# Performance work log

Hardware: AMD Instinct MI355X
Metric: run time of the kernel (lower is better)

The kernel has to match this reference:

```python
import jax, jax.numpy as jnp
import numpy as np

P = 32      # process_dim (event types)
H = 1024    # hidden_size
T = 128     # sequence length
B = 128     # batch size


def setup_inputs() -> dict:
    key = jax.random.key(0)
    k_dt, k_ty, k_e, k_w, k_b = jax.random.split(key, 5)
    seq_dt = jax.random.uniform(k_dt, (T, B), dtype=jnp.float32)
    seq_types = jax.random.randint(k_ty, (T, B), 0, P, dtype=jnp.int32)
    h0 = jnp.zeros((B, H), jnp.float32)
    c0 = jnp.zeros((B, H), jnp.float32)
    # Embedding: P+1 rows, padding row (index P) zeroed as in nn.Embedding(padding_idx=P)
    embed = (jax.random.normal(k_e, (P + 1, P), jnp.float32) * 0.02).at[P].set(0.0)
    # 7 gate Linears fused into one weight: order = [input, forget, output,
    # input_target, forget_target, z, decay]; torch Linear is y = v @ W^T + b,
    # here W is stored pre-transposed as [P+H, 7H].
    W = jax.random.normal(k_w, (P + H, 7 * H), jnp.float32) / np.sqrt(P + H)
    b = jax.random.normal(k_b, (7 * H,), jnp.float32) * 0.01
    return {"seq_dt": seq_dt, "seq_types": seq_types, "h0": h0, "c0": c0,
            "embed": embed, "W": W, "b": b}


def reference(seq_dt, seq_types, h0, c0, embed, W, b):
    def step(carry, inp):
        h_t, c_t, c_tgt = carry
        dt, types = inp                       # dt: [B], types: [B]
        x = embed[types]                      # [B, P]
        v = jnp.concatenate([x, h_t], axis=1) # [B, P+H]
        g = v @ W + b                         # fused 7-gate GEMM -> [B, 7H]
        gi, gf, go, git, gft, gz, gd = jnp.split(g, 7, axis=1)
        inpt = jax.nn.sigmoid(gi)
        forget = jax.nn.sigmoid(gf)
        output = jax.nn.sigmoid(go)
        in_tgt = jax.nn.sigmoid(git)
        fg_tgt = jax.nn.sigmoid(gft)
        z = jnp.tanh(gz)
        decay = jax.nn.softplus(8.0 * gd) / 8.0  # Softplus(beta=8)
        c_i = forget * c_t + inpt * z
        h_i = output * jnp.tanh(c_i)
        c_tgt_new = fg_tgt * c_tgt + in_tgt * z
        c_new = c_tgt_new + (c_i - c_tgt_new) * jnp.exp(-decay * dt[:, None])
        h_new = output * jnp.tanh(c_new)
        return (h_new, c_new, c_tgt_new), (h_i, h_new, output, c_i, c_tgt_new, decay)

    _, ys = jax.lax.scan(step, (h0, c0, c0), (seq_dt, seq_types))
    hiddens, hiddens_decayed, outputs, cells, cell_targets, decays = ys
    return hiddens, hiddens_decayed, outputs, cells, cell_targets, decays
```

## Files before the change

### kernel.cpp

```cpp
#include <hip/hip_runtime.h>
#include <hip/hip_bf16.h>

#define TT 128
#define BB 128
#define HH 1024
#define PP 32
#define G7 7168

typedef __attribute__((ext_vector_type(8))) short short8;
typedef __attribute__((ext_vector_type(4))) float f32x4;

__device__ __forceinline__ ushort f2bf(float f) {
    union { float f; unsigned int u; } v; v.f = f;
    unsigned int u = v.u;
    return (ushort)((u + 0x7FFFu + ((u >> 16) & 1u)) >> 16);
}
__device__ __forceinline__ float sigm(float x) { return 1.f / (1.f + __expf(-x)); }
__device__ __forceinline__ float ftanh(float x) {
    float e = __expf(2.f * x);
    return 1.f - 2.f / (e + 1.f);
}

__global__ void prep_w2(const float* __restrict__ W, ushort* __restrict__ W2) {
    int nt = blockIdx.x;
    int ki = blockIdx.y;
    int lane = threadIdx.x;
    int n = nt * 16 + (lane & 15);
    int k = ki * 32 + (lane >> 4) * 8;
    size_t off = ((size_t)(nt * 32 + ki) * 64 + lane) * 8;
    #pragma unroll
    for (int e = 0; e < 8; ++e)
        W2[off + e] = f2bf(W[(size_t)(32 + k + e) * G7 + n]);
}

__global__ void prep_g0(const float* __restrict__ W, const float* __restrict__ embed,
                        const float* __restrict__ bias, float* __restrict__ G0) {
    int n = blockIdx.x * 256 + threadIdx.x;
    int ty = blockIdx.y;
    float acc = bias[n];
    for (int p = 0; p < PP; ++p)
        acc += embed[ty * PP + p] * W[(size_t)p * G7 + n];
    G0[(size_t)ty * G7 + n] = acc;
}

__global__ void prep_init(const float* __restrict__ h0, const float* __restrict__ c0,
                          ushort* __restrict__ A4, float* __restrict__ c_state,
                          float* __restrict__ ctgt_state) {
    int i = blockIdx.x * 256 + threadIdx.x;
    int b = i >> 10, k = i & 1023;
    int lane = (b & 15) | (((k >> 3) & 3) << 4);
    size_t off = ((size_t)(((b >> 5) * 32 + (k >> 5)) * 2 + ((b >> 4) & 1)) * 64 + lane) * 8 + (k & 7);
    A4[off] = f2bf(h0[i]);
    c_state[i] = c0[i];
    ctgt_state[i] = c0[i];
}

__global__ __launch_bounds__(896) void step_kernel(
    const ushort* __restrict__ W2, const float* __restrict__ G0,
    const float* __restrict__ dts, const int* __restrict__ types,
    const ushort* __restrict__ a_read, ushort* __restrict__ a_write,
    float* __restrict__ c_state, float* __restrict__ ctgt_state,
    float* __restrict__ out, int t)
{
    __shared__ short8 Albuf[4096];
    __shared__ f32x4 pbuf[7][2][64];
    __shared__ float gbuf[7][32][16];
    const int tid = threadIdx.x;
    const int wave = tid >> 6, lane = tid & 63;
    const int g = wave >> 1, kh = wave & 1;
    const int bid = blockIdx.x;
    const int ht = (bid & 7) * 8 + ((bid >> 3) & 7);
    const int bq = bid >> 6;

    const short8* Asrc = reinterpret_cast<const short8*>(a_read) + bq * 4096;
    #pragma unroll
    for (int r = 0; r < 4; ++r)
        Albuf[r * 896 + tid] = Asrc[r * 896 + tid];
    if (tid < 512) Albuf[3584 + tid] = Asrc[3584 + tid];
    __syncthreads();

    const short8* Wv = reinterpret_cast<const short8*>(W2)
                     + (size_t)(g * 64 + ht) * 2048 + (kh * 16) * 64 + lane;
    const short8* As = Albuf + (kh * 16) * 2 * 64 + lane;
    f32x4 acc0 = {}, acc1 = {};
    #pragma unroll 8
    for (int j = 0; j < 16; ++j) {
        short8 wf = Wv[j * 64];
        short8 a0 = As[(j * 2 + 0) * 64];
        short8 a1 = As[(j * 2 + 1) * 64];
        acc0 = __builtin_amdgcn_mfma_f32_16x16x32_bf16(a0, wf, acc0, 0, 0, 0);
        acc1 = __builtin_amdgcn_mfma_f32_16x16x32_bf16(a1, wf, acc1, 0, 0, 0);
    }

    if (kh == 1) { pbuf[g][0][lane] = acc0; pbuf[g][1][lane] = acc1; }
    __syncthreads();
    if (kh == 0) {
        acc0 += pbuf[g][0][lane];
        acc1 += pbuf[g][1][lane];
        const int rb = (lane >> 4) * 4, lr = lane & 15;
        #pragma unroll
        for (int r = 0; r < 4; ++r) {
            gbuf[g][rb + r][lr]      = acc0[r];
            gbuf[g][16 + rb + r][lr] = acc1[r];
        }
    }
    __syncthreads();

    if (tid < 512) {
        const int br = tid >> 4, hc = tid & 15;
        const int b = bq * 32 + br;
        const int h = ht * 16 + hc;
        const int ty = types[t * BB + b];
        const float dt = dts[t * BB + b];
        const float* g0p = G0 + (size_t)ty * G7 + h;
        float pre[7];
        #pragma unroll
        for (int gg = 0; gg < 7; ++gg)
            pre[gg] = gbuf[gg][br][hc] + g0p[gg * HH];

        float inpt   = sigm(pre[0]);
        float forget = sigm(pre[1]);
        float output = sigm(pre[2]);
        float itg    = sigm(pre[3]);
        float ftg    = sigm(pre[4]);
        float z      = ftanh(pre[5]);
        float x8     = 8.f * pre[6];
        float sp     = fmaxf(x8, 0.f) + __logf(1.f + __expf(-fabsf(x8)));
        float decay  = sp * 0.125f;

        const size_t si = (size_t)b * HH + h;
        float c    = c_state[si];
        float ctgt = ctgt_state[si];
        float c_i      = forget * c + inpt * z;
        float h_i      = output * ftanh(c_i);
        float ctgt_new = ftg * ctgt + itg * z;
        float edt      = __expf(-decay * dt);
        float c_new    = ctgt_new + (c_i - ctgt_new) * edt;
        float h_new    = output * ftanh(c_new);

        const size_t OS = (size_t)TT * BB * HH;
        size_t ob = (size_t)t * BB * HH + si;
        __builtin_nontemporal_store(h_i,      &out[ob]);
        __builtin_nontemporal_store(h_new,    &out[OS + ob]);
        __builtin_nontemporal_store(output,   &out[2 * OS + ob]);
        __builtin_nontemporal_store(c_i,      &out[3 * OS + ob]);
        __builtin_nontemporal_store(ctgt_new, &out[4 * OS + ob]);
        __builtin_nontemporal_store(decay,    &out[5 * OS + ob]);
        c_state[si]    = c_new;
        ctgt_state[si] = ctgt_new;
        int ki_w = h >> 5;
        int lane_w = (b & 15) | (((h >> 3) & 3) << 4);
        size_t aoff = ((size_t)((((b >> 5) * 32 + ki_w) * 2 + ((b >> 4) & 1)) * 64) + lane_w) * 8 + (h & 7);
        a_write[aoff] = f2bf(h_new);
    }
}

extern "C" void kernel_launch(void* const* d_in, const int* in_sizes, int n_in,
                              void* d_out, int out_size, void* d_ws, size_t ws_size,
                              hipStream_t stream) {
    const float* seq_dt    = (const float*)d_in[0];
    const int*   seq_types = (const int*)d_in[1];
    const float* h0        = (const float*)d_in[2];
    const float* c0        = (const float*)d_in[3];
    const float* embed     = (const float*)d_in[4];
    const float* W         = (const float*)d_in[5];
    const float* bias      = (const float*)d_in[6];
    float* out = (float*)d_out;

    char* ws = (char*)d_ws;
    ushort* W2  = (ushort*)ws;
    float*  G0b = (float*)(ws + 14680064);
    ushort* a40 = (ushort*)(ws + 15626240);
    ushort* a41 = (ushort*)(ws + 15888384);
    float*  cs  = (float*)(ws + 16150528);
    float*  cts = (float*)(ws + 16674816);

    hipLaunchKernelGGL(prep_w2, dim3(448, 32), dim3(64), 0, stream, W, W2);
    hipLaunchKernelGGL(prep_g0, dim3(28, 33), dim3(256), 0, stream, W, embed, bias, G0b);
    hipLaunchKernelGGL(prep_init, dim3(512), dim3(256), 0, stream, h0, c0, a40, cs, cts);

    for (int t = 0; t < TT; ++t) {
        const ushort* ar = (t & 1) ? a41 : a40;
        ushort*       aw = (t & 1) ? a40 : a41;
        hipLaunchKernelGGL(step_kernel, dim3(256), dim3(896), 0, stream,
                           W2, G0b, seq_dt, seq_types, ar, aw, cs, cts, out, t);
    }
}
```

Before: 842.6 us.

## Pipeline A-tile and weight loads in chunks, drop separate ctgt state buffer

Splits the per-step GEMM into four K-chunks, prefetching the next chunk of the shared-memory A tile and the weight fragments into registers while MFMAs run on the current chunk, so global loads overlap with compute. It removes the separate cell-target state buffer and reads the previous step's ctgt back from the output tensor, which is now written with a normal store so it stays in cache. It also pads the gate buffer in shared memory to avoid bank conflicts. This costs three extra barriers per step and more register pressure.

```diff
diff --git a/kernel.cpp b/kernel.cpp
--- a/kernel.cpp
+++ b/kernel.cpp
@@ -44,27 +44,25 @@
 }
 
 __global__ void prep_init(const float* __restrict__ h0, const float* __restrict__ c0,
-                          ushort* __restrict__ A4, float* __restrict__ c_state,
-                          float* __restrict__ ctgt_state) {
+                          ushort* __restrict__ A4, float* __restrict__ c_state) {
     int i = blockIdx.x * 256 + threadIdx.x;
     int b = i >> 10, k = i & 1023;
     int lane = (b & 15) | (((k >> 3) & 3) << 4);
     size_t off = ((size_t)(((b >> 5) * 32 + (k >> 5)) * 2 + ((b >> 4) & 1)) * 64 + lane) * 8 + (k & 7);
     A4[off] = f2bf(h0[i]);
     c_state[i] = c0[i];
-    ctgt_state[i] = c0[i];
 }
 
 __global__ __launch_bounds__(896) void step_kernel(
     const ushort* __restrict__ W2, const float* __restrict__ G0,
     const float* __restrict__ dts, const int* __restrict__ types,
+    const float* __restrict__ c0,
     const ushort* __restrict__ a_read, ushort* __restrict__ a_write,
-    float* __restrict__ c_state, float* __restrict__ ctgt_state,
-    float* __restrict__ out, int t)
+    float* __restrict__ c_state, float* __restrict__ out, int t)
 {
     __shared__ short8 Albuf[4096];
     __shared__ f32x4 pbuf[7][2][64];
-    __shared__ float gbuf[7][32][16];
+    __shared__ float gbuf[7][32][17];
     const int tid = threadIdx.x;
     const int wave = tid >> 6, lane = tid & 63;
     const int g = wave >> 1, kh = wave & 1;
@@ -73,23 +71,40 @@
     const int bq = bid >> 6;
 
     const short8* Asrc = reinterpret_cast<const short8*>(a_read) + bq * 4096;
+    const short8* Wv = reinterpret_cast<const short8*>(W2)
+                     + (size_t)(g * 64 + ht) * 2048 + lane;
+
+    Albuf[tid] = Asrc[tid];
+    if (tid < 128) Albuf[896 + tid] = Asrc[896 + tid];
+    short8 wr0[4], wr1[4];
     #pragma unroll
-    for (int r = 0; r < 4; ++r)
-        Albuf[r * 896 + tid] = Asrc[r * 896 + tid];
-    if (tid < 512) Albuf[3584 + tid] = Asrc[3584 + tid];
+    for (int j = 0; j < 4; ++j)
+        wr0[j] = Wv[(kh + 2 * j) * 64];
     __syncthreads();
 
-    const short8* Wv = reinterpret_cast<const short8*>(W2)
-                     + (size_t)(g * 64 + ht) * 2048 + (kh * 16) * 64 + lane;
-    const short8* As = Albuf + (kh * 16) * 2 * 64 + lane;
     f32x4 acc0 = {}, acc1 = {};
-    #pragma unroll 8
-    for (int j = 0; j < 16; ++j) {
-        short8 wf = Wv[j * 64];
-        short8 a0 = As[(j * 2 + 0) * 64];
-        short8 a1 = As[(j * 2 + 1) * 64];
-        acc0 = __builtin_amdgcn_mfma_f32_16x16x32_bf16(a0, wf, acc0, 0, 0, 0);
-        acc1 = __builtin_amdgcn_mfma_f32_16x16x32_bf16(a1, wf, acc1, 0, 0, 0);
+    #pragma unroll
+    for (int c = 0; c < 4; ++c) {
+        if (c < 3) {
+            Albuf[(c + 1) * 1024 + tid] = Asrc[(c + 1) * 1024 + tid];
+            if (tid < 128)
+                Albuf[(c + 1) * 1024 + 896 + tid] = Asrc[(c + 1) * 1024 + 896 + tid];
+            #pragma unroll
+            for (int j = 0; j < 4; ++j)
+                wr1[j] = Wv[((c + 1) * 8 + kh + 2 * j) * 64];
+        }
+        const short8* As = Albuf + c * 1024 + lane;
+        #pragma unroll
+        for (int j = 0; j < 4; ++j) {
+            const int kloc = kh + 2 * j;
+            short8 a0 = As[(kloc * 2 + 0) * 64];
+            short8 a1 = As[(kloc * 2 + 1) * 64];
+            acc0 = __builtin_amdgcn_mfma_f32_16x16x32_bf16(a0, wr0[j], acc0, 0, 0, 0);
+            acc1 = __builtin_amdgcn_mfma_f32_16x16x32_bf16(a1, wr0[j], acc1, 0, 0, 0);
+        }
+        __syncthreads();
+        #pragma unroll
+        for (int j = 0; j < 4; ++j) wr0[j] = wr1[j];
     }
 
     if (kh == 1) { pbuf[g][0][lane] = acc0; pbuf[g][1][lane] = acc1; }
@@ -129,8 +144,9 @@
         float decay  = sp * 0.125f;
 
         const size_t si = (size_t)b * HH + h;
+        const size_t OS = (size_t)TT * BB * HH;
         float c    = c_state[si];
-        float ctgt = ctgt_state[si];
+        float ctgt = (t == 0) ? c0[si] : out[4 * OS + (size_t)(t - 1) * BB * HH + si];
         float c_i      = forget * c + inpt * z;
         float h_i      = output * ftanh(c_i);
         float ctgt_new = ftg * ctgt + itg * z;
@@ -138,16 +154,14 @@
         float c_new    = ctgt_new + (c_i - ctgt_new) * edt;
         float h_new    = output * ftanh(c_new);
 
-        const size_t OS = (size_t)TT * BB * HH;
         size_t ob = (size_t)t * BB * HH + si;
         __builtin_nontemporal_store(h_i,      &out[ob]);
         __builtin_nontemporal_store(h_new,    &out[OS + ob]);
         __builtin_nontemporal_store(output,   &out[2 * OS + ob]);
         __builtin_nontemporal_store(c_i,      &out[3 * OS + ob]);
-        __builtin_nontemporal_store(ctgt_new, &out[4 * OS + ob]);
+        out[4 * OS + ob] = ctgt_new;
         __builtin_nontemporal_store(decay,    &out[5 * OS + ob]);
-        c_state[si]    = c_new;
-        ctgt_state[si] = ctgt_new;
+        c_state[si] = c_new;
         int ki_w = h >> 5;
         int lane_w = (b & 15) | (((h >> 3) & 3) << 4);
         size_t aoff = ((size_t)((((b >> 5) * 32 + ki_w) * 2 + ((b >> 4) & 1)) * 64) + lane_w) * 8 + (h & 7);
@@ -173,16 +187,15 @@
     ushort* a40 = (ushort*)(ws + 15626240);
     ushort* a41 = (ushort*)(ws + 15888384);
     float*  cs  = (float*)(ws + 16150528);
-    float*  cts = (float*)(ws + 16674816);
 
     hipLaunchKernelGGL(prep_w2, dim3(448, 32), dim3(64), 0, stream, W, W2);
     hipLaunchKernelGGL(prep_g0, dim3(28, 33), dim3(256), 0, stream, W, embed, bias, G0b);
-    hipLaunchKernelGGL(prep_init, dim3(512), dim3(256), 0, stream, h0, c0, a40, cs, cts);
+    hipLaunchKernelGGL(prep_init, dim3(512), dim3(256), 0, stream, h0, c0, a40, cs);
 
     for (int t = 0; t < TT; ++t) {
         const ushort* ar = (t & 1) ? a41 : a40;
         ushort*       aw = (t & 1) ? a40 : a41;
         hipLaunchKernelGGL(step_kernel, dim3(256), dim3(896), 0, stream,
-                           W2, G0b, seq_dt, seq_types, ar, aw, cs, cts, out, t);
-    }
-}
+                           W2, G0b, seq_dt, seq_types, c0, ar, aw, cs, out, t);
+    }
+}
```

Measured after the change: 927.7 us. +10.1%, slower.
